# Kernel tuning notes

Hardware: AMD Instinct MI355X
Metric: run time of the kernel (lower is better)

The kernel has to match this reference:

```python
import jax, jax.numpy as jnp
import numpy as np

B, S, D, H = 2, 2048, 1024, 16
HD = D // H


def setup_inputs() -> dict:
    key = jax.random.key(0)
    ks = jax.random.split(key, 5)
    x = jax.random.normal(ks[0], (B, S, D), dtype=jnp.float32)
    qk_w = jax.random.normal(ks[1], (D, 2 * D), dtype=jnp.float32) * 0.02
    qk_b = jnp.zeros((2 * D,), dtype=jnp.float32)
    v_w = jax.random.normal(ks[2], (D, D), dtype=jnp.float32) * 0.02
    cproj_w = jax.random.normal(ks[3], (D, D), dtype=jnp.float32) * 0.02
    resid_gain = jnp.ones((1, H, 1, 1), dtype=jnp.float32)
    skip_gain = jnp.ones((1, H, 1, 1), dtype=jnp.float32)
    centre_gain = jnp.ones((1, H, 1, 1), dtype=jnp.float32)
    return {"x": x, "qk_w": qk_w, "qk_b": qk_b, "v_w": v_w,
            "cproj_w": cproj_w, "resid_gain": resid_gain,
            "skip_gain": skip_gain, "centre_gain": centre_gain}


def reference(x, qk_w, qk_b, v_w, cproj_w, resid_gain, skip_gain, centre_gain):
    b, s, d = x.shape
    h, hd = H, d // H
    # fused QK projection (pconv with bias)
    qk = x @ qk_w + qk_b                      # [B,S,2D]
    q, k = jnp.split(qk, 2, axis=-1)
    v = x @ v_w                               # [B,S,D] (pconv, bias=0)
    # split heads -> [B,H,S,hd]
    q = q.reshape(b, s, h, hd).transpose(0, 2, 1, 3)
    k = k.reshape(b, s, h, hd).transpose(0, 2, 1, 3)
    v = v.reshape(b, s, h, hd).transpose(0, 2, 1, 3)
    # scaled QK^T with causal mask
    scores = jnp.einsum('bhqd,bhkd->bhqk', q, k) / jnp.sqrt(jnp.float32(hd))
    causal = jnp.tril(jnp.ones((s, s), dtype=bool))
    neg = jnp.finfo(scores.dtype).min
    scores = jnp.where(causal, scores, neg)
    attn = jax.nn.softmax(scores, axis=-1)    # [B,H,S,S]
    # shaped attention: per-head resid gain + skip (identity) - centred uniform causal
    row = jnp.arange(1, s + 1, dtype=jnp.float32)
    uniform = jnp.tril(jnp.ones((s, s), dtype=jnp.float32) / row[:, None])  # [S,S]
    eye = jnp.eye(s, dtype=jnp.float32)
    new_attn = (resid_gain * attn
                + skip_gain * eye[None, None]
                - centre_gain * uniform[None, None])
    out = jnp.einsum('bhqk,bhkd->bhqd', new_attn, v)  # [B,H,S,hd]
    out = out.transpose(0, 2, 1, 3).reshape(b, s, d)  # merge heads
    out = out @ cproj_w                                # c_proj (bias=0)
    return out
```

## Files before the change

### kernel.cpp

```cpp
#include <hip/hip_runtime.h>
#include <hip/hip_bf16.h>


typedef __hip_bfloat16 bf16;
typedef short s16x8 __attribute__((ext_vector_type(8)));
typedef short s16x4 __attribute__((ext_vector_type(4)));
typedef float f32x4 __attribute__((ext_vector_type(4)));

#define NB 2
#define NS 2048
#define ND 1024
#define NH 16
#define NHD 64
#define QSCALE 0.18033688011112042f
#define THR 8.0f
#define SW(r) (((r) & 7) << 4)

__device__ __forceinline__ float b2f(unsigned short u) {
  union { float f; unsigned int i; } c; c.i = ((unsigned int)u) << 16; return c.f;
}

__device__ __forceinline__ unsigned short f2bu(float f) {
  bf16 t = __float2bfloat16(f);
  unsigned short u;
  __builtin_memcpy(&u, &t, 2);
  return u;
}

__device__ __forceinline__ void gload_lds16(const void* g, void* l) {
  __builtin_amdgcn_global_load_lds((const __attribute__((address_space(1))) void*)g,
                                   (__attribute__((address_space(3))) void*)l, 16, 0, 0);
}

__global__ __launch_bounds__(256) void prologue(const float* __restrict__ x,
                                                const float* __restrict__ qk_w,
                                                const float* __restrict__ v_w,
                                                const float* __restrict__ cp_w,
                                                bf16* __restrict__ xb,
                                                bf16* __restrict__ qkwt,
                                                bf16* __restrict__ vwt,
                                                bf16* __restrict__ cpwt) {
  const int z = blockIdx.z;
  const int tx = threadIdx.x, ty = threadIdx.y;
  if (z == 0) {
    const int lb = (int)blockIdx.x + 64 * (int)blockIdx.y;
    const int base = lb * 2048 + (ty * 32 + tx) * 8;
    float4 v0 = *(const float4*)(x + base);
    float4 v1 = *(const float4*)(x + base + 4);
    ushort4 o0, o1;
    o0.x = f2bu(v0.x); o0.y = f2bu(v0.y); o0.z = f2bu(v0.z); o0.w = f2bu(v0.w);
    o1.x = f2bu(v1.x); o1.y = f2bu(v1.y); o1.z = f2bu(v1.z); o1.w = f2bu(v1.w);
    *(ushort4*)(xb + base) = o0;
    *(ushort4*)(xb + base + 4) = o1;
    return;
  }
  const int N = (z == 1) ? 2048 : 1024;
  if ((int)blockIdx.x * 32 >= N) return;
  const float* in = (z == 1) ? qk_w : (z == 2) ? v_w : cp_w;
  bf16* out = (z == 1) ? qkwt : (z == 2) ? vwt : cpwt;
  const int K = 1024;
  __shared__ float tile[32][33];
  int nt = blockIdx.x * 32, kt = blockIdx.y * 32;
#pragma unroll
  for (int j = 0; j < 32; j += 8)
    tile[ty + j][tx] = in[(size_t)(kt + ty + j) * N + nt + tx];
  __syncthreads();
#pragma unroll
  for (int j = 0; j < 32; j += 8)
    out[(size_t)(nt + ty + j) * K + kt + tx] = __float2bfloat16(tile[tx][ty + j]);
}

__global__ __launch_bounds__(256) void gemm_qkv(const bf16* __restrict__ A,
                                                const bf16* __restrict__ BtQK,
                                                const bf16* __restrict__ BtV,
                                                const float* __restrict__ bias,
                                                bf16* __restrict__ qo, bf16* __restrict__ ko,
                                                bf16* __restrict__ vo) {
  __shared__ alignas(16) bf16 As[128 * 32];
  __shared__ alignas(16) bf16 Bs[128 * 32];
  const int K = 1024;
  const int tid = threadIdx.x;
  const int wave = tid >> 6, lane = tid & 63;
  const int l15 = lane & 15, lg = lane >> 4;
  const int wr = wave >> 1, wc = wave & 1;
  const int brow = blockIdx.y * 128, bcol = blockIdx.x * 128;
  const bf16* Bsrc = (bcol < 2048) ? (BtQK + (size_t)bcol * K)
                                   : (BtV + (size_t)(bcol - 2048) * K);

  f32x4 acc[4][4] = {};
  const int r0 = tid >> 2;
  const int kc = (tid & 3) * 8;
  char* AsB = (char*)As;
  char* BsB = (char*)Bs;

  for (int k0 = 0; k0 < K; k0 += 32) {
    gload_lds16(A + (size_t)(brow + r0) * K + k0 + kc, AsB + tid * 16);
    gload_lds16(A + (size_t)(brow + r0 + 64) * K + k0 + kc, AsB + 4096 + tid * 16);
    gload_lds16(Bsrc + (size_t)r0 * K + k0 + kc, BsB + tid * 16);
    gload_lds16(Bsrc + (size_t)(r0 + 64) * K + k0 + kc, BsB + 4096 + tid * 16);
    __syncthreads();
    s16x8 af[4], bfr[4];
#pragma unroll
    for (int mi = 0; mi < 4; ++mi)
      af[mi] = *(const s16x8*)(As + (wr * 64 + mi * 16 + l15) * 32 + lg * 8);
#pragma unroll
    for (int ni = 0; ni < 4; ++ni)
      bfr[ni] = *(const s16x8*)(Bs + (wc * 64 + ni * 16 + l15) * 32 + lg * 8);
#pragma unroll
    for (int mi = 0; mi < 4; ++mi)
#pragma unroll
      for (int ni = 0; ni < 4; ++ni)
        acc[mi][ni] = __builtin_amdgcn_mfma_f32_16x16x32_bf16(af[mi], bfr[ni], acc[mi][ni], 0, 0, 0);
    __syncthreads();
  }

#pragma unroll
  for (int mi = 0; mi < 4; ++mi)
#pragma unroll
    for (int ni = 0; ni < 4; ++ni)
#pragma unroll
      for (int r = 0; r < 4; ++r) {
        int row = brow + wr * 64 + mi * 16 + lg * 4 + r;
        int col = bcol + wc * 64 + ni * 16 + l15;
        float v = acc[mi][ni][r];
        int b = row >> 11, s = row & 2047;
        int cc = col & 1023;
        int h = cc >> 6, e = cc & 63;
        if (col < 1024) {
          v = (v + bias[col]) * QSCALE;
          qo[((((size_t)b * NH + h) * NS) + s) * NHD + e] = __float2bfloat16(v);
        } else if (col < 2048) {
          v += bias[col];
          ko[((((size_t)b * NH + h) * NS) + s) * NHD + e] = __float2bfloat16(v);
        } else {
          vo[((((size_t)b * NH + h) * NHD) + e) * NS + s] = __float2bfloat16(v);
        }
      }
}

__global__ __launch_bounds__(256) void gemm_out(const bf16* __restrict__ A,
                                                const bf16* __restrict__ Bt,
                                                float* __restrict__ of) {
  __shared__ alignas(16) bf16 As[128 * 32];
  __shared__ alignas(16) bf16 Bs[64 * 32];
  const int K = 1024, N = 1024;
  const int tid = threadIdx.x;
  const int wave = tid >> 6, lane = tid & 63;
  const int l15 = lane & 15, lg = lane >> 4;
  const int brow = blockIdx.y * 128, bcol = blockIdx.x * 64;

  f32x4 acc[2][4] = {};
  const int r0 = tid >> 2;
  const int kc = (tid & 3) * 8;
  char* AsB = (char*)As;
  char* BsB = (char*)Bs;

  for (int k0 = 0; k0 < K; k0 += 32) {
    gload_lds16(A + (size_t)(brow + r0) * K + k0 + kc, AsB + tid * 16);
    gload_lds16(A + (size_t)(brow + r0 + 64) * K + k0 + kc, AsB + 4096 + tid * 16);
    gload_lds16(Bt + (size_t)(bcol + r0) * K + k0 + kc, BsB + tid * 16);
    __syncthreads();
    s16x8 af[2], bfr[4];
#pragma unroll
    for (int mi = 0; mi < 2; ++mi)
      af[mi] = *(const s16x8*)(As + (wave * 32 + mi * 16 + l15) * 32 + lg * 8);
#pragma unroll
    for (int ni = 0; ni < 4; ++ni)
      bfr[ni] = *(const s16x8*)(Bs + (ni * 16 + l15) * 32 + lg * 8);
#pragma unroll
    for (int mi = 0; mi < 2; ++mi)
#pragma unroll
      for (int ni = 0; ni < 4; ++ni)
        acc[mi][ni] = __builtin_amdgcn_mfma_f32_16x16x32_bf16(af[mi], bfr[ni], acc[mi][ni], 0, 0, 0);
    __syncthreads();
  }

#pragma unroll
  for (int mi = 0; mi < 2; ++mi)
#pragma unroll
    for (int ni = 0; ni < 4; ++ni)
#pragma unroll
      for (int r = 0; r < 4; ++r) {
        int row = brow + wave * 32 + mi * 16 + lg * 4 + r;
        int col = bcol + ni * 16 + l15;
        of[(size_t)row * N + col] = acc[mi][ni][r];
      }
}

__global__ __launch_bounds__(256, 4) void attn_kernel(const bf16* __restrict__ qb,
                                                      const bf16* __restrict__ kb,
                                                      const bf16* __restrict__ vtb,
                                                      const float* __restrict__ rg,
                                                      const float* __restrict__ sg,
                                                      const float* __restrict__ cg,
                                                      bf16* __restrict__ out) {
  const int hb = blockIdx.x;
  const int h = hb & 15, b = hb >> 4;
  const int qt = 31 - (int)blockIdx.y;
  const int tid = threadIdx.x, wave = tid >> 6, lane = tid & 63;
  const int l15 = lane & 15, lg = lane >> 4;

  __shared__ alignas(16) char Ks[2][64 * 128];
  __shared__ alignas(16) char Vs[2][64 * 128];
  __shared__ alignas(16) char Pl[4][2048];
  char* Plw = Pl[wave];
  const int swz = ((((l15 >> 3) ^ l15) & 7) << 4);

  const size_t hoff = ((size_t)b * NH + h) * NS * NHD;
  const bf16* Q = qb + hoff;
  const bf16* K = kb + hoff;
  const bf16* VT = vtb + hoff;
  const float rgh = rg[h], sgh = sg[h], cgh = cg[h];

  const int qbase = qt * 64 + wave * 16;
  const int qloc = wave * 16 + l15;

  s16x8 qa0 = *(const s16x8*)(Q + (size_t)(qbase + l15) * NHD + lg * 8);
  s16x8 qa1 = *(const s16x8*)(Q + (size_t)(qbase + l15) * NHD + 32 + lg * 8);

  const short ONE = 0x3F80;
  const s16x8 ones = {ONE, ONE, ONE, ONE, ONE, ONE, ONE, ONE};
  s16x8 pc0, pc1;
#pragma unroll
  for (int j = 0; j < 8; ++j) {
    pc0[j] = (lg * 8 + j <= qloc) ? ONE : (short)0;
    pc1[j] = (32 + lg * 8 + j <= qloc) ? ONE : (short)0;
  }

  f32x4 acc_o[4] = {};
  f32x4 acc_c[4] = {};
  float m_run = -INFINITY, l_run = 0.f;

  const int srow = tid >> 3;
  const int sce = (tid & 7) * 8;
  const int scb0 = (sce * 2) ^ SW(srow);
  const int scb1 = (sce * 2) ^ SW(srow + 32);

  s16x8 kra = *(const s16x8*)(K + (size_t)srow * NHD + sce);
  s16x8 krb = *(const s16x8*)(K + (size_t)(srow + 32) * NHD + sce);
  s16x8 vra = *(const s16x8*)(VT + (size_t)srow * NS + sce);
  s16x8 vrb = *(const s16x8*)(VT + (size_t)(srow + 32) * NS + sce);

  for (int t = 0; t <= qt; ++t) {
    const bool diag = (t == qt);
    char* Kb = Ks[t & 1];
    char* Vb = Vs[t & 1];
    *(s16x8*)(Kb + srow * 128 + scb0) = kra;
    *(s16x8*)(Kb + (srow + 32) * 128 + scb1) = krb;
    *(s16x8*)(Vb + srow * 128 + scb0) = vra;
    *(s16x8*)(Vb + (srow + 32) * 128 + scb1) = vrb;
    if (t < qt) {
      const bf16* Kn = K + (size_t)(t + 1) * 64 * NHD;
      const bf16* Vn = VT + (t + 1) * 64;
      kra = *(const s16x8*)(Kn + (size_t)srow * NHD + sce);
      krb = *(const s16x8*)(Kn + (size_t)(srow + 32) * NHD + sce);
      vra = *(const s16x8*)(Vn + (size_t)srow * NS + sce);
      vrb = *(const s16x8*)(Vn + (size_t)(srow + 32) * NS + sce);
    }
    __syncthreads();

    f32x4 sc[4] = {};
    __builtin_amdgcn_s_setprio(1);
#pragma unroll
    for (int c = 0; c < 4; ++c) {
      const int R = c * 16 + l15;
      s16x8 kf0 = *(const s16x8*)(Kb + R * 128 + ((lg * 16) ^ SW(R)));
      s16x8 kf1 = *(const s16x8*)(Kb + R * 128 + ((64 + lg * 16) ^ SW(R)));
      sc[c] = __builtin_amdgcn_mfma_f32_16x16x32_bf16(kf0, qa0, sc[c], 0, 0, 0);
      sc[c] = __builtin_amdgcn_mfma_f32_16x16x32_bf16(kf1, qa1, sc[c], 0, 0, 0);
    }
    __builtin_amdgcn_s_setprio(0);

    if (diag) {
#pragma unroll
      for (int c = 0; c < 4; ++c)
#pragma unroll
        for (int r = 0; r < 4; ++r)
          if (c * 16 + lg * 4 + r > qloc) sc[c][r] = -INFINITY;
    }

    float mxc[4];
#pragma unroll
    for (int c = 0; c < 4; ++c)
      mxc[c] = fmaxf(fmaxf(sc[c][0], sc[c][1]), fmaxf(sc[c][2], sc[c][3]));
    float mx = fmaxf(fmaxf(mxc[0], mxc[1]), fmaxf(mxc[2], mxc[3]));
    mx = fmaxf(mx, __shfl_xor(mx, 16, 64));
    mx = fmaxf(mx, __shfl_xor(mx, 32, 64));

    const bool grow = !__all(mx <= m_run + THR);
    float m_new = grow ? fmaxf(m_run, mx) : m_run;

    float p[4][4];
    float rs = 0.f;
#pragma unroll
    for (int c = 0; c < 4; ++c)
#pragma unroll
      for (int r = 0; r < 4; ++r) {
        float e = exp2f(sc[c][r] - m_new);
        p[c][r] = e;
        rs += e;
      }
    rs += __shfl_xor(rs, 16, 64);
    rs += __shfl_xor(rs, 32, 64);

    if (grow) {
      float cr = exp2f(m_run - m_new);
      l_run = l_run * cr + rs;
      m_run = m_new;
      float crr[4];
#pragma unroll
      for (int r = 0; r < 4; ++r) crr[r] = __shfl(cr, lg * 4 + r, 64);
#pragma unroll
      for (int sub = 0; sub < 4; ++sub)
#pragma unroll
        for (int r = 0; r < 4; ++r) acc_o[sub][r] *= crr[r];
    } else {
      l_run += rs;
    }

#pragma unroll
    for (int c = 0; c < 4; ++c) {
      s16x4 pk;
      pk[0] = (short)f2bu(p[c][0]);
      pk[1] = (short)f2bu(p[c][1]);
      pk[2] = (short)f2bu(p[c][2]);
      pk[3] = (short)f2bu(p[c][3]);
      *(s16x4*)(Plw + l15 * 128 + ((c * 32 + lg * 8) ^ swz)) = pk;
    }
    s16x8 pa0 = *(const s16x8*)(Plw + l15 * 128 + ((lg * 16) ^ swz));
    s16x8 pa1 = *(const s16x8*)(Plw + l15 * 128 + ((64 + lg * 16) ^ swz));

    const s16x8 qc0 = diag ? pc0 : ones;
    const s16x8 qc1 = diag ? pc1 : ones;

    __builtin_amdgcn_s_setprio(1);
#pragma unroll
    for (int sub = 0; sub < 4; ++sub) {
      const int Rv = sub * 16 + l15;
      s16x8 vf0 = *(const s16x8*)(Vb + Rv * 128 + ((lg * 16) ^ SW(Rv)));
      s16x8 vf1 = *(const s16x8*)(Vb + Rv * 128 + ((64 + lg * 16) ^ SW(Rv)));
      acc_o[sub] = __builtin_amdgcn_mfma_f32_16x16x32_bf16(pa0, vf0, acc_o[sub], 0, 0, 0);
      acc_o[sub] = __builtin_amdgcn_mfma_f32_16x16x32_bf16(pa1, vf1, acc_o[sub], 0, 0, 0);
      acc_c[sub] = __builtin_amdgcn_mfma_f32_16x16x32_bf16(qc0, vf0, acc_c[sub], 0, 0, 0);
      acc_c[sub] = __builtin_amdgcn_mfma_f32_16x16x32_bf16(qc1, vf1, acc_c[sub], 0, 0, 0);
    }
    __builtin_amdgcn_s_setprio(0);
  }

  const char* Vd = Vs[qt & 1];
  float linv[4];
#pragma unroll
  for (int r = 0; r < 4; ++r) linv[r] = 1.0f / __shfl(l_run, lg * 4 + r, 64);

#pragma unroll
  for (int sub = 0; sub < 4; ++sub) {
    const int d = sub * 16 + l15;
    const int cb = wave * 32 + lg * 8;
    s16x4 vr4 = *(const s16x4*)(Vd + d * 128 + (cb ^ SW(d)));
    unsigned short vbits[4];
    __builtin_memcpy(vbits, &vr4, 8);
#pragma unroll
    for (int r = 0; r < 4; ++r) {
      int q = qbase + lg * 4 + r;
      float val = rgh * acc_o[sub][r] * linv[r] + sgh * b2f(vbits[r]) -
                  cgh * acc_c[sub][r] / (float)(q + 1);
      out[((size_t)b * NS + q) * ND + h * NHD + d] = __float2bfloat16(val);
    }
  }
}

extern "C" void kernel_launch(void* const* d_in, const int* in_sizes, int n_in,
                              void* d_out, int out_size, void* d_ws, size_t ws_size,
                              hipStream_t stream) {
  const float* x = (const float*)d_in[0];
  const float* qk_w = (const float*)d_in[1];
  const float* qk_b = (const float*)d_in[2];
  const float* v_w = (const float*)d_in[3];
  const float* cproj_w = (const float*)d_in[4];
  const float* rg = (const float*)d_in[5];
  const float* sg = (const float*)d_in[6];
  const float* cg = (const float*)d_in[7];
  float* out = (float*)d_out;

  char* p = (char*)d_ws;
  bf16* xb = (bf16*)p;   p += (size_t)4096 * 1024 * 2;
  bf16* qkwt = (bf16*)p; p += (size_t)2048 * 1024 * 2;
  bf16* vwt = (bf16*)p;  p += (size_t)1024 * 1024 * 2;
  bf16* cpwt = (bf16*)p; p += (size_t)1024 * 1024 * 2;
  bf16* qbuf = (bf16*)p; p += (size_t)NB * NH * NS * NHD * 2;
  bf16* kbuf = (bf16*)p; p += (size_t)NB * NH * NS * NHD * 2;
  bf16* vtbuf = (bf16*)p; p += (size_t)NB * NH * NS * NHD * 2;
  bf16* aout = (bf16*)p; p += (size_t)4096 * 1024 * 2;

  prologue<<<dim3(64, 32, 4), dim3(32, 8), 0, stream>>>(x, qk_w, v_w, cproj_w,
                                                        xb, qkwt, vwt, cpwt);
  gemm_qkv<<<dim3(24, 32), 256, 0, stream>>>(xb, qkwt, vwt, qk_b, qbuf, kbuf, vtbuf);
  attn_kernel<<<dim3(32, 32), 256, 0, stream>>>(qbuf, kbuf, vtbuf, rg, sg, cg, aout);
  gemm_out<<<dim3(16, 32), 256, 0, stream>>>(aout, cpwt, out);
}
```

Measured before the change: 129.0 us.

## Pair short and long causal query tiles in one 512-thread attention block

Each attention block now holds two 4-wave groups, one working on query tile j and one on tile 31-j. They share the K/V tiles staged in LDS, with each thread loading one row instead of two. This evens out causal work across blocks and halves the grid. The short-tile group finishes early and then only helps with loads and barriers, and the 512-thread blocks may cut occupancy.

```diff
diff --git a/kernel.cpp b/kernel.cpp
--- a/kernel.cpp
+++ b/kernel.cpp
@@ -187,7 +187,7 @@
       }
 }
 
-__global__ __launch_bounds__(256, 4) void attn_kernel(const bf16* __restrict__ qb,
+__global__ __launch_bounds__(512, 4) void attn_kernel(const bf16* __restrict__ qb,
                                                       const bf16* __restrict__ kb,
                                                       const bf16* __restrict__ vtb,
                                                       const float* __restrict__ rg,
@@ -196,13 +196,16 @@
                                                       bf16* __restrict__ out) {
   const int hb = blockIdx.x;
   const int h = hb & 15, b = hb >> 4;
-  const int qt = 31 - (int)blockIdx.y;
+  const int j = blockIdx.y;
   const int tid = threadIdx.x, wave = tid >> 6, lane = tid & 63;
   const int l15 = lane & 15, lg = lane >> 4;
+  const int grp = wave >> 2, wv4 = wave & 3;
+  const int qt = grp ? (31 - j) : j;
+  const int ntm1 = 31 - j;
 
   __shared__ alignas(16) char Ks[2][64 * 128];
   __shared__ alignas(16) char Vs[2][64 * 128];
-  __shared__ alignas(16) char Pl[4][2048];
+  __shared__ alignas(16) char Pl[8][2048];
   char* Plw = Pl[wave];
   const int swz = ((((l15 >> 3) ^ l15) & 7) << 4);
 
@@ -212,8 +215,8 @@
   const bf16* VT = vtb + hoff;
   const float rgh = rg[h], sgh = sg[h], cgh = cg[h];
 
-  const int qbase = qt * 64 + wave * 16;
-  const int qloc = wave * 16 + l15;
+  const int qbase = qt * 64 + wv4 * 16;
+  const int qloc = wv4 * 16 + l15;
 
   s16x8 qa0 = *(const s16x8*)(Q + (size_t)(qbase + l15) * NHD + lg * 8);
   s16x8 qa1 = *(const s16x8*)(Q + (size_t)(qbase + l15) * NHD + 32 + lg * 8);
@@ -222,9 +225,9 @@
   const s16x8 ones = {ONE, ONE, ONE, ONE, ONE, ONE, ONE, ONE};
   s16x8 pc0, pc1;
 #pragma unroll
-  for (int j = 0; j < 8; ++j) {
-    pc0[j] = (lg * 8 + j <= qloc) ? ONE : (short)0;
-    pc1[j] = (32 + lg * 8 + j <= qloc) ? ONE : (short)0;
+  for (int jj = 0; jj < 8; ++jj) {
+    pc0[jj] = (lg * 8 + jj <= qloc) ? ONE : (short)0;
+    pc1[jj] = (32 + lg * 8 + jj <= qloc) ? ONE : (short)0;
   }
 
   f32x4 acc_o[4] = {};
@@ -233,31 +236,24 @@
 
   const int srow = tid >> 3;
   const int sce = (tid & 7) * 8;
-  const int scb0 = (sce * 2) ^ SW(srow);
-  const int scb1 = (sce * 2) ^ SW(srow + 32);
+  const int scb = (sce * 2) ^ SW(srow);
 
   s16x8 kra = *(const s16x8*)(K + (size_t)srow * NHD + sce);
-  s16x8 krb = *(const s16x8*)(K + (size_t)(srow + 32) * NHD + sce);
   s16x8 vra = *(const s16x8*)(VT + (size_t)srow * NS + sce);
-  s16x8 vrb = *(const s16x8*)(VT + (size_t)(srow + 32) * NS + sce);
-
-  for (int t = 0; t <= qt; ++t) {
-    const bool diag = (t == qt);
+
+  for (int t = 0; t <= ntm1; ++t) {
     char* Kb = Ks[t & 1];
     char* Vb = Vs[t & 1];
-    *(s16x8*)(Kb + srow * 128 + scb0) = kra;
-    *(s16x8*)(Kb + (srow + 32) * 128 + scb1) = krb;
-    *(s16x8*)(Vb + srow * 128 + scb0) = vra;
-    *(s16x8*)(Vb + (srow + 32) * 128 + scb1) = vrb;
-    if (t < qt) {
-      const bf16* Kn = K + (size_t)(t + 1) * 64 * NHD;
-      const bf16* Vn = VT + (t + 1) * 64;
-      kra = *(const s16x8*)(Kn + (size_t)srow * NHD + sce);
-      krb = *(const s16x8*)(Kn + (size_t)(srow + 32) * NHD + sce);
-      vra = *(const s16x8*)(Vn + (size_t)srow * NS + sce);
-      vrb = *(const s16x8*)(Vn + (size_t)(srow + 32) * NS + sce);
-    }
-    __syncthreads();
+    *(s16x8*)(Kb + srow * 128 + scb) = kra;
+    *(s16x8*)(Vb + srow * 128 + scb) = vra;
+    if (t < ntm1) {
+      kra = *(const s16x8*)(K + ((size_t)(t + 1) * 64 + srow) * NHD + sce);
+      vra = *(const s16x8*)(VT + (size_t)srow * NS + (t + 1) * 64 + sce);
+    }
+    __syncthreads();
+
+    if (t > qt) continue;
+    const bool diag = (t == qt);
 
     f32x4 sc[4] = {};
     __builtin_amdgcn_s_setprio(1);
@@ -345,26 +341,26 @@
       acc_c[sub] = __builtin_amdgcn_mfma_f32_16x16x32_bf16(qc1, vf1, acc_c[sub], 0, 0, 0);
     }
     __builtin_amdgcn_s_setprio(0);
-  }
-
-  const char* Vd = Vs[qt & 1];
-  float linv[4];
-#pragma unroll
-  for (int r = 0; r < 4; ++r) linv[r] = 1.0f / __shfl(l_run, lg * 4 + r, 64);
-
-#pragma unroll
-  for (int sub = 0; sub < 4; ++sub) {
-    const int d = sub * 16 + l15;
-    const int cb = wave * 32 + lg * 8;
-    s16x4 vr4 = *(const s16x4*)(Vd + d * 128 + (cb ^ SW(d)));
-    unsigned short vbits[4];
-    __builtin_memcpy(vbits, &vr4, 8);
-#pragma unroll
-    for (int r = 0; r < 4; ++r) {
-      int q = qbase + lg * 4 + r;
-      float val = rgh * acc_o[sub][r] * linv[r] + sgh * b2f(vbits[r]) -
-                  cgh * acc_c[sub][r] / (float)(q + 1);
-      out[((size_t)b * NS + q) * ND + h * NHD + d] = __float2bfloat16(val);
+
+    if (diag) {
+      float linv[4];
+#pragma unroll
+      for (int r = 0; r < 4; ++r) linv[r] = 1.0f / __shfl(l_run, lg * 4 + r, 64);
+#pragma unroll
+      for (int sub = 0; sub < 4; ++sub) {
+        const int d = sub * 16 + l15;
+        const int cb = wv4 * 32 + lg * 8;
+        s16x4 vr4 = *(const s16x4*)(Vb + d * 128 + (cb ^ SW(d)));
+        unsigned short vbits[4];
+        __builtin_memcpy(vbits, &vr4, 8);
+#pragma unroll
+        for (int r = 0; r < 4; ++r) {
+          int q = qbase + lg * 4 + r;
+          float val = rgh * acc_o[sub][r] * linv[r] + sgh * b2f(vbits[r]) -
+                      cgh * acc_c[sub][r] / (float)(q + 1);
+          out[((size_t)b * NS + q) * ND + h * NHD + d] = __float2bfloat16(val);
+        }
+      }
     }
   }
 }
@@ -395,6 +391,6 @@
   prologue<<<dim3(64, 32, 4), dim3(32, 8), 0, stream>>>(x, qk_w, v_w, cproj_w,
                                                         xb, qkwt, vwt, cpwt);
   gemm_qkv<<<dim3(24, 32), 256, 0, stream>>>(xb, qkwt, vwt, qk_b, qbuf, kbuf, vtbuf);
-  attn_kernel<<<dim3(32, 32), 256, 0, stream>>>(qbuf, kbuf, vtbuf, rg, sg, cg, aout);
+  attn_kernel<<<dim3(32, 16), 512, 0, stream>>>(qbuf, kbuf, vtbuf, rg, sg, cg, aout);
   gemm_out<<<dim3(16, 32), 256, 0, stream>>>(aout, cpwt, out);
 }
```

Result: no change. 126.9 us (-1.7%).
